# Optimization experiments

Measured on AMD Instinct MI355X. Metric: run time of the kernel, lower is better.

The kernel has to match this reference:

```python
import jax, jax.numpy as jnp
import numpy as np

B, L, DM, H, DK, DV, DH = 16, 1024, 512, 8, 64, 64, 2048
FACTOR = 5
EPS = 1e-5


def _ln(x, g, b):
    m = x.mean(-1, keepdims=True)
    v = jnp.mean((x - m) ** 2, axis=-1, keepdims=True)
    return g * (x - m) / jnp.sqrt(v + EPS) + b


def setup_inputs() -> dict:
    key = jax.random.key(0)
    ks = jax.random.split(key, 12)
    w = lambda k, s: jax.random.normal(k, s, jnp.float32) * 0.02
    sample_k = min(FACTOR * int(np.ceil(np.log(L))), L)  # 35
    return {
        "x": jax.random.normal(ks[0], (B, L, DM), jnp.float32),
        "Wq": w(ks[1], (DM, H * DK)), "bq": jnp.zeros((H * DK,), jnp.float32),
        "Wk": w(ks[2], (DM, H * DK)), "bk": jnp.zeros((H * DK,), jnp.float32),
        "Wv": w(ks[3], (DM, H * DV)), "bv": jnp.zeros((H * DV,), jnp.float32),
        "Wo": w(ks[4], (H * DV, DM)), "bo": jnp.zeros((DM,), jnp.float32),
        "g1": jnp.ones((DM,), jnp.float32), "beta1": jnp.zeros((DM,), jnp.float32),
        "W1": w(ks[5], (DM, DH)), "bf1": jnp.zeros((DH,), jnp.float32),
        "W2": w(ks[6], (DH, DM)), "bf2": jnp.zeros((DM,), jnp.float32),
        "g2": jnp.ones((DM,), jnp.float32), "beta2": jnp.zeros((DM,), jnp.float32),
        "index_sample": jax.random.randint(ks[7], (L, sample_k), 0, L),
        "stage": 0,  # eval; mask=False so attn_mask is always False
    }


def _prob_attention(Q, K, V, index_sample):
    # Q,K,V: [B,H,L,D] (Informer ProbAttention, mask_flag=False, eval)
    Bq, Hq, Lq, D = Q.shape
    u = index_sample.shape[1]  # u == U_part since L_Q == L_K
    # sparse sampled scores: K gathered per-query -> [B,H,L,sample_k,D]
    K_sample = K[:, :, index_sample, :]
    QK_sample = jnp.einsum("bhld,bhlsd->bhls", Q, K_sample)
    M = QK_sample.max(-1) - QK_sample.mean(-1)            # [B,H,L] sparsity measure
    _, M_top = jax.lax.top_k(M, u)                         # [B,H,u]
    Q_reduce = jnp.take_along_axis(Q, M_top[..., None], axis=2)  # [B,H,u,D]
    scores = jnp.einsum("bhud,bhld->bhul", Q_reduce, K) / jnp.sqrt(jnp.float32(D))
    attn = jax.nn.softmax(scores, axis=-1)                 # [B,H,u,L]
    # initial context = mean of V over keys, broadcast to all queries
    context = jnp.broadcast_to(V.mean(axis=2, keepdims=True), V.shape)
    bi = jnp.arange(Bq)[:, None, None]
    hi = jnp.arange(Hq)[None, :, None]
    context = context.at[bi, hi, M_top].set(jnp.einsum("bhul,bhld->bhud", attn, V))
    # output_attention=True: uniform 1/L everywhere, true attn at selected queries
    attns = jnp.full((Bq, Hq, Lq, Lq), 1.0 / Lq, dtype=attn.dtype)
    attns = attns.at[bi, hi, M_top].set(attn)
    return context, attns


def reference(x, Wq, bq, Wk, bk, Wv, bv, Wo, bo, g1, beta1, W1, bf1, W2, bf2, g2, beta2, index_sample, stage):
    residual = x
    Q = (x @ Wq + bq).reshape(B, L, H, DK).transpose(0, 2, 1, 3)
    K = (x @ Wk + bk).reshape(B, L, H, DK).transpose(0, 2, 1, 3)
    V = (x @ Wv + bv).reshape(B, L, H, DV).transpose(0, 2, 1, 3)
    ctx, score = _prob_attention(Q, K, V, index_sample)
    ctx = ctx.transpose(0, 2, 1, 3).reshape(B, L, H * DV)
    out = ctx @ Wo + bo
    x1 = _ln(out + residual, g1, beta1)          # dropout = identity (eval)
    ffn = jax.nn.relu(x1 @ W1 + bf1) @ W2 + bf2
    x2 = _ln(ffn + x1, g2, beta2)
    return x2, score
```

## Files before the change

kernel.cpp:

```cpp
#include <hip/hip_runtime.h>
#include <cstdint>
#include <cstddef>

#define Bc 16
#define Lc 1024
#define DMc 512
#define Hc 8
#define DHc 2048
#define Uc 35

typedef __attribute__((ext_vector_type(8))) short bf16x8;
typedef __attribute__((ext_vector_type(4))) float f32x4;

__device__ __forceinline__ ushort f2bf(float f) {
    union { float f; uint32_t u; } v; v.f = f;
    uint32_t r = v.u + 0x7FFF + ((v.u >> 16) & 1);
    return (ushort)(r >> 16);
}
__device__ __forceinline__ float bf2f(ushort u) {
    union { uint32_t i; float f; } v; v.i = ((uint32_t)u) << 16; return v.f;
}

__device__ __forceinline__ void glds16(const ushort* g, ushort* l) {
    __builtin_amdgcn_global_load_lds(
        (__attribute__((address_space(1))) void*)(void*)const_cast<ushort*>(g),
        (__attribute__((address_space(3))) void*)l, 16, 0, 0);
}

template<int MODE>
__global__ __launch_bounds__(256) void gemm_mfma(
    const ushort* __restrict__ A, const ushort* __restrict__ Bt,
    const float* __restrict__ bias, void* __restrict__ out0,
    void* __restrict__ out1, int M, int N, int K, int nxb)
{
    __shared__ ushort As[2][128 * 64];
    __shared__ ushort Bs[2][128 * 64];
    const int nwg = gridDim.x;
    int wg = blockIdx.x;
    wg = (wg & 7) * (nwg >> 3) + (wg >> 3);
    const int n0 = (wg % nxb) * 128;
    const int m0 = (wg / nxb) * 128;

    const int tid = threadIdx.x;
    const int lane = tid & 63;
    const int wave = tid >> 6;
    const int wr = wave >> 1, wc = wave & 1;
    const int lrow = lane & 15;
    const int lk = (lane >> 4) * 8;

    f32x4 zero = {0.f, 0.f, 0.f, 0.f};
    f32x4 acc[4][4];
    #pragma unroll
    for (int m = 0; m < 4; ++m)
        #pragma unroll
        for (int n = 0; n < 4; ++n) acc[m][n] = zero;

    const int srow = tid >> 3;
    const int skc = (tid & 7) * 8;
    const int ldsb = (tid & 192) * 8;

    auto stage = [&](int k0, int bufi) {
        #pragma unroll
        for (int r = 0; r < 4; ++r) {
            glds16(A  + (size_t)(m0 + r * 32 + srow) * K + k0 + skc, &As[bufi][r * 2048 + ldsb]);
            glds16(Bt + (size_t)(n0 + r * 32 + srow) * K + k0 + skc, &Bs[bufi][r * 2048 + ldsb]);
        }
    };

    const int nt = K >> 6;
    stage(0, 0);
    __syncthreads();
    int cur = 0;
    for (int t = 0; t < nt; ++t) {
        if (t + 1 < nt) stage((t + 1) << 6, cur ^ 1);
        #pragma unroll
        for (int kk = 0; kk < 2; ++kk) {
            bf16x8 af[4], bv[4];
            #pragma unroll
            for (int m = 0; m < 4; ++m)
                af[m] = *reinterpret_cast<const bf16x8*>(&As[cur][(wr * 64 + m * 16 + lrow) * 64 + kk * 32 + lk]);
            #pragma unroll
            for (int n = 0; n < 4; ++n)
                bv[n] = *reinterpret_cast<const bf16x8*>(&Bs[cur][(wc * 64 + n * 16 + lrow) * 64 + kk * 32 + lk]);
            #pragma unroll
            for (int m = 0; m < 4; ++m)
                #pragma unroll
                for (int n = 0; n < 4; ++n)
                    acc[m][n] = __builtin_amdgcn_mfma_f32_16x16x32_bf16(af[m], bv[n], acc[m][n], 0, 0, 0);
        }
        __syncthreads();
        cur ^= 1;
    }

    #pragma unroll
    for (int n = 0; n < 4; ++n) {
        int col = n0 + wc * 64 + n * 16 + lrow;
        float bval = bias[col];
        #pragma unroll
        for (int m = 0; m < 4; ++m) {
            #pragma unroll
            for (int j = 0; j < 4; ++j) {
                int row = m0 + wr * 64 + m * 16 + (lane >> 4) * 4 + j;
                float v = acc[m][n][j] + bval;
                if (MODE == 2) v = fmaxf(v, 0.0f);
                if (MODE == 0)
                    ((float*)out0)[(size_t)row * N + col] = v;
                else if (MODE == 1 || MODE == 2)
                    ((ushort*)out0)[(size_t)row * N + col] = f2bf(v);
                else {
                    if (col < 1024) ((ushort*)out0)[(size_t)row * 1024 + col] = f2bf(v);
                    else            ((float*)out1)[(size_t)row * 512 + (col - 1024)] = v;
                }
            }
        }
    }
}

__device__ __forceinline__ void tr_tile(
    const float* __restrict__ in, ushort* __restrict__ out,
    int K, int N, int bx, int by, float (*t)[33], int tid)
{
    int n0 = bx * 32, k0 = by * 32;
    int tx = tid & 31, ty = tid >> 5;
    #pragma unroll
    for (int dy = 0; dy < 32; dy += 8)
        t[ty + dy][tx] = in[(size_t)(k0 + ty + dy) * N + n0 + tx];
    __syncthreads();
    #pragma unroll
    for (int dy = 0; dy < 32; dy += 8)
        out[(size_t)(n0 + ty + dy) * K + k0 + tx] = f2bf(t[tx][ty + dy]);
}

#define PREP_BLKS (8192 + 4 * 256 + 2 * 1024 + 1)
#define FILL_BLKS 32768

__global__ __launch_bounds__(256) void prep_kernel(
    const float* __restrict__ x,
    const float* __restrict__ Wq, const float* __restrict__ Wk,
    const float* __restrict__ Wv, const float* __restrict__ Wo,
    const float* __restrict__ W1, const float* __restrict__ W2,
    const float* __restrict__ bq, const float* __restrict__ bk,
    const float* __restrict__ bv,
    ushort* __restrict__ xbf, ushort* __restrict__ Wqkvt,
    ushort* __restrict__ Wot, ushort* __restrict__ W1t,
    ushort* __restrict__ W2t, float* __restrict__ bcat,
    float* __restrict__ score_out)
{
    __shared__ float t[32][33];
    const int tid = threadIdx.x;
    int bid = blockIdx.x;
    if (bid < 8192) {
        int i = bid * 256 + tid;
        float4 v = reinterpret_cast<const float4*>(x)[i];
        uint32_t lo = (uint32_t)f2bf(v.x) | ((uint32_t)f2bf(v.y) << 16);
        uint32_t hi = (uint32_t)f2bf(v.z) | ((uint32_t)f2bf(v.w) << 16);
        reinterpret_cast<uint2*>(xbf)[i] = make_uint2(lo, hi);
        return;
    }
    bid -= 8192;
    if (bid < 256) { tr_tile(Wq, Wqkvt,              512, 512, bid & 15, bid >> 4, t, tid); return; }
    bid -= 256;
    if (bid < 256) { tr_tile(Wk, Wqkvt + 512 * 512,  512, 512, bid & 15, bid >> 4, t, tid); return; }
    bid -= 256;
    if (bid < 256) { tr_tile(Wv, Wqkvt + 1024 * 512, 512, 512, bid & 15, bid >> 4, t, tid); return; }
    bid -= 256;
    if (bid < 256) { tr_tile(Wo, Wot,                512, 512, bid & 15, bid >> 4, t, tid); return; }
    bid -= 256;
    if (bid < 1024) { tr_tile(W1, W1t,               512, 2048, bid & 63, bid >> 6, t, tid); return; }
    bid -= 1024;
    if (bid < 1024) { tr_tile(W2, W2t,               2048, 512, bid & 15, bid >> 4, t, tid); return; }
    bid -= 1024;
    if (bid < 1) {
        for (int i = tid; i < 1536; i += 256)
            bcat[i] = (i < 512) ? bq[i] : (i < 1024) ? bk[i - 512] : bv[i - 1024];
        return;
    }
    bid -= 1;
    const float iv = 1.0f / (float)Lc;
    float4 v = make_float4(iv, iv, iv, iv);
    size_t i = (size_t)bid * 256 + tid;
    const size_t nthreads = (size_t)FILL_BLKS * 256;
    float4* p = reinterpret_cast<float4*>(score_out);
    #pragma unroll
    for (int c = 0; c < 4; ++c) p[i + c * nthreads] = v;
}

__global__ __launch_bounds__(256) void compute_M_kernel(
    const ushort* __restrict__ QK, const int* __restrict__ idx,
    float* __restrict__ Mout)
{
    __shared__ float qs[4][64];
    const int tid = threadIdx.x;
    const int wid = tid >> 6;
    const int lane = tid & 63;
    const int task = blockIdx.x * 4 + wid;
    const int l = task & (Lc - 1);
    const int bh = task >> 10;
    const int h = bh & (Hc - 1);
    const int b = bh >> 3;

    qs[wid][lane] = bf2f(QK[(size_t)(b * Lc + l) * 1024 + h * 64 + lane]);

    const bool act = lane < Uc;
    int kl = act ? idx[l * Uc + lane] : 0;
    const bf16x8* kr = reinterpret_cast<const bf16x8*>(
        QK + (size_t)(b * Lc + kl) * 1024 + 512 + h * 64);
    float dot = 0.0f;
    if (act) {
        #pragma unroll
        for (int c = 0; c < 8; ++c) {
            bf16x8 kv = kr[c];
            #pragma unroll
            for (int e = 0; e < 8; ++e)
                dot += qs[wid][c * 8 + e] * bf2f((ushort)kv[e]);
        }
    }
    float mx = act ? dot : -INFINITY;
    float sm = act ? dot : 0.0f;
    #pragma unroll
    for (int off = 32; off; off >>= 1) {
        mx = fmaxf(mx, __shfl_xor(mx, off, 64));
        sm += __shfl_xor(sm, off, 64);
    }
    if (lane == 0) Mout[task] = mx - sm * (1.0f / Uc);
}

__global__ __launch_bounds__(256) void topk_kernel(
    const float* __restrict__ Mvals, int* __restrict__ Mtop)
{
    const int bh = blockIdx.x;
    const int t = threadIdx.x;
    const int lane = t & 63, wid = t >> 6;
    float v[4];
    #pragma unroll
    for (int c = 0; c < 4; ++c) v[c] = Mvals[((size_t)bh << 10) + t + 256 * c];

    __shared__ float cv[4];
    __shared__ int   ci[4];
    __shared__ int   wini;

    for (int j = 0; j < Uc; ++j) {
        float bv = v[0]; int bi = t;
        #pragma unroll
        for (int c = 1; c < 4; ++c)
            if (v[c] > bv) { bv = v[c]; bi = t + 256 * c; }
        #pragma unroll
        for (int off = 32; off; off >>= 1) {
            float ov = __shfl_xor(bv, off, 64);
            int   oi = __shfl_xor(bi, off, 64);
            if (ov > bv || (ov == bv && oi < bi)) { bv = ov; bi = oi; }
        }
        if (lane == 0) { cv[wid] = bv; ci[wid] = bi; }
        __syncthreads();
        if (t == 0) {
            float fv = cv[0]; int fi = ci[0];
            #pragma unroll
            for (int w = 1; w < 4; ++w)
                if (cv[w] > fv || (cv[w] == fv && ci[w] < fi)) { fv = cv[w]; fi = ci[w]; }
            Mtop[bh * Uc + j] = fi;
            wini = fi;
        }
        __syncthreads();
        int wi = wini;
        if ((wi & 255) == t) v[wi >> 8] = -INFINITY;
    }
}

__global__ __launch_bounds__(256) void qk_scores_kernel(
    const ushort* __restrict__ QK, const int* __restrict__ Mtop,
    float* __restrict__ score)
{
    const int bh = blockIdx.x >> 2;
    const int l0 = (blockIdx.x & 3) * 256;
    const int h = bh & (Hc - 1), b = bh >> 3;
    __shared__ int qpos[Uc];
    __shared__ float Qs[Uc][64];
    const int t = threadIdx.x;
    if (t < Uc) qpos[t] = Mtop[bh * Uc + t];
    __syncthreads();
    for (int i = t; i < Uc * 64; i += 256) {
        int j = i >> 6, d = i & 63;
        Qs[j][d] = bf2f(QK[(size_t)(b * Lc + qpos[j]) * 1024 + h * 64 + d]);
    }
    __syncthreads();

    const int l = l0 + t;
    const bf16x8* kr = reinterpret_cast<const bf16x8*>(
        QK + (size_t)(b * Lc + l) * 1024 + 512 + h * 64);
    float acc[Uc] = {};
    #pragma unroll
    for (int c = 0; c < 8; ++c) {
        bf16x8 kv = kr[c];
        float kf[8];
        #pragma unroll
        for (int e = 0; e < 8; ++e) kf[e] = bf2f((ushort)kv[e]);
        #pragma unroll
        for (int j = 0; j < Uc; ++j) {
            float s = 0.0f;
            #pragma unroll
            for (int e = 0; e < 8; ++e) s += Qs[j][c * 8 + e] * kf[e];
            acc[j] += s;
        }
    }
    #pragma unroll
    for (int j = 0; j < Uc; ++j)
        score[((size_t)(bh << 10) + qpos[j]) * Lc + l] = acc[j] * 0.125f;
}

__global__ __launch_bounds__(256) void attn_out_kernel(
    float* __restrict__ score, const float* __restrict__ V,
    const int* __restrict__ Mtop, ushort* __restrict__ ctx)
{
    const int bh = blockIdx.x;
    const int h = bh & (Hc - 1), b = bh >> 3;
    const int t = threadIdx.x;
    const int d = t & 63, part = t >> 6;

    __shared__ int qpos[Uc];
    __shared__ float mz[Uc][2];
    __shared__ float buf[4][Uc][64];
    __shared__ float vmred[4][64];
    __shared__ float vmf[64];

    if (t < Uc) qpos[t] = Mtop[bh * Uc + t];
    __syncthreads();

    for (int j = part; j < Uc; j += 4) {
        const float* row = score + ((size_t)(bh << 10) + qpos[j]) * Lc;
        float v[16];
        float mx = -INFINITY;
        #pragma unroll
        for (int c = 0; c < 16; ++c) { v[c] = row[c * 64 + d]; mx = fmaxf(mx, v[c]); }
        #pragma unroll
        for (int off = 32; off; off >>= 1) mx = fmaxf(mx, __shfl_xor(mx, off, 64));
        float z = 0.0f;
        #pragma unroll
        for (int c = 0; c < 16; ++c) z += expf(v[c] - mx);
        #pragma unroll
        for (int off = 32; off; off >>= 1) z += __shfl_xor(z, off, 64);
        if (d == 0) { mz[j][0] = mx; mz[j][1] = 1.0f / z; }
    }
    __syncthreads();

    float acc[Uc];
    #pragma unroll
    for (int j = 0; j < Uc; ++j) acc[j] = 0.0f;
    float vm = 0.0f;

    for (int c = 0; c < 4; ++c) {
        const int l0 = part * 256 + c * 64;
        #pragma unroll
        for (int j = 0; j < Uc; ++j) {
            size_t off = ((size_t)(bh << 10) + qpos[j]) * Lc + l0 + d;
            float p = expf(score[off] - mz[j][0]) * mz[j][1];
            buf[part][j][d] = p;
            score[off] = p;
        }
        __syncthreads();
        #pragma unroll 4
        for (int li = 0; li < 64; ++li) {
            float v = V[((size_t)(b << 10) + l0 + li) * 512 + h * 64 + d];
            vm += v;
            #pragma unroll
            for (int j = 0; j < Uc; ++j) acc[j] += buf[part][j][li] * v;
        }
        __syncthreads();
    }

    #pragma unroll
    for (int j = 0; j < Uc; ++j) buf[part][j][d] = acc[j];
    vmred[part][d] = vm;
    __syncthreads();
    if (t < 64) vmf[t] = (vmred[0][t] + vmred[1][t] + vmred[2][t] + vmred[3][t]) * (1.0f / Lc);
    __syncthreads();

    const int dcol = (t & 15) * 4;
    ushort4 vmu;
    vmu.x = f2bf(vmf[dcol + 0]); vmu.y = f2bf(vmf[dcol + 1]);
    vmu.z = f2bf(vmf[dcol + 2]); vmu.w = f2bf(vmf[dcol + 3]);
    for (int li = 0; li < 64; ++li) {
        int l = (t >> 4) + li * 16;
        *reinterpret_cast<ushort4*>(ctx + ((size_t)(b << 10) + l) * 512 + h * 64 + dcol) = vmu;
    }
    __syncthreads();

    for (int idx = t; idx < Uc * 64; idx += 256) {
        int j = idx >> 6, d2 = idx & 63;
        float s = buf[0][j][d2] + buf[1][j][d2] + buf[2][j][d2] + buf[3][j][d2];
        ctx[((size_t)(b << 10) + qpos[j]) * 512 + h * 64 + d2] = f2bf(s);
    }
}

template<int A_BF, int B_BF, int OUT_BF>
__global__ __launch_bounds__(256) void ln_kernel(
    const void* __restrict__ a, const void* __restrict__ bsrc,
    const float* __restrict__ g, const float* __restrict__ beta,
    void* __restrict__ y)
{
    const int row = blockIdx.x;
    const int t = threadIdx.x;
    float a0, a1, b0, b1;
    if (A_BF) {
        uint32_t u = ((const uint32_t*)a)[(size_t)row * 256 + t];
        a0 = bf2f((ushort)(u & 0xffff)); a1 = bf2f((ushort)(u >> 16));
    } else {
        float2 f = ((const float2*)a)[(size_t)row * 256 + t];
        a0 = f.x; a1 = f.y;
    }
    if (B_BF) {
        uint32_t u = ((const uint32_t*)bsrc)[(size_t)row * 256 + t];
        b0 = bf2f((ushort)(u & 0xffff)); b1 = bf2f((ushort)(u >> 16));
    } else {
        float2 f = ((const float2*)bsrc)[(size_t)row * 256 + t];
        b0 = f.x; b1 = f.y;
    }
    float v0 = a0 + b0, v1 = a1 + b1;
    __shared__ float red[256];
    red[t] = v0 + v1; __syncthreads();
    for (int s = 128; s; s >>= 1) { if (t < s) red[t] += red[t + s]; __syncthreads(); }
    float mean = red[0] * (1.0f / DMc);
    __syncthreads();
    float d0 = v0 - mean, d1 = v1 - mean;
    red[t] = d0 * d0 + d1 * d1; __syncthreads();
    for (int s = 128; s; s >>= 1) { if (t < s) red[t] += red[t + s]; __syncthreads(); }
    float inv = rsqrtf(red[0] * (1.0f / DMc) + 1e-5f);
    float2 gv = ((const float2*)g)[t];
    float2 bt = ((const float2*)beta)[t];
    float o0 = gv.x * d0 * inv + bt.x;
    float o1 = gv.y * d1 * inv + bt.y;
    if (OUT_BF) {
        uint32_t u = (uint32_t)f2bf(o0) | ((uint32_t)f2bf(o1) << 16);
        ((uint32_t*)y)[(size_t)row * 256 + t] = u;
    } else {
        ((float2*)y)[(size_t)row * 256 + t] = make_float2(o0, o1);
    }
}

extern "C" void kernel_launch(void* const* d_in, const int* in_sizes, int n_in,
                              void* d_out, int out_size, void* d_ws, size_t ws_size,
                              hipStream_t stream)
{
    const float* x     = (const float*)d_in[0];
    const float* Wq    = (const float*)d_in[1];
    const float* bq    = (const float*)d_in[2];
    const float* Wk    = (const float*)d_in[3];
    const float* bk    = (const float*)d_in[4];
    const float* Wv    = (const float*)d_in[5];
    const float* bv    = (const float*)d_in[6];
    const float* Wo    = (const float*)d_in[7];
    const float* bo    = (const float*)d_in[8];
    const float* g1    = (const float*)d_in[9];
    const float* beta1 = (const float*)d_in[10];
    const float* W1    = (const float*)d_in[11];
    const float* bf1   = (const float*)d_in[12];
    const float* W2    = (const float*)d_in[13];
    const float* bf2   = (const float*)d_in[14];
    const float* g2    = (const float*)d_in[15];
    const float* beta2 = (const float*)d_in[16];
    const int* index_sample = (const int*)d_in[17];

    const size_t NTOK = (size_t)Bc * Lc;
    const size_t QKV_SZ = NTOK * DMc;
    const size_t HID_SZ = NTOK * DHc;

    char* p = (char*)d_ws;
    auto alloc = [&](size_t bytes) { char* r = p; p += (bytes + 255) & ~(size_t)255; return r; };
    ushort* QKbf   = (ushort*)alloc(NTOK * 1024 * 2);
    float*  V      = (float*) alloc(QKV_SZ * 4);
    ushort* hidden = (ushort*)alloc(HID_SZ * 2);
    ushort* xbf    = (ushort*)alloc(QKV_SZ * 2);
    ushort* ctxbf  = (ushort*)alloc(QKV_SZ * 2);
    ushort* x1bf   = (ushort*)alloc(QKV_SZ * 2);
    ushort* projbf = (ushort*)alloc(QKV_SZ * 2);
    float*  ffnf   = (float*) alloc(QKV_SZ * 4);
    ushort* Wqkvt  = (ushort*)alloc((size_t)1536 * 512 * 2);
    ushort* Wot    = (ushort*)alloc((size_t)512 * 512 * 2);
    ushort* W1t    = (ushort*)alloc((size_t)512 * 2048 * 2);
    ushort* W2t    = (ushort*)alloc((size_t)512 * 2048 * 2);
    float*  bcat   = (float*) alloc(1536 * 4);
    float*  Mbuf   = (float*) alloc((size_t)Bc * Hc * Lc * 4);
    int*    Mtop   = (int*)   alloc((size_t)Bc * Hc * 64 * 4);

    float* x2_out    = (float*)d_out;
    float* score_out = x2_out + QKV_SZ;

    dim3 blk(256);

    prep_kernel<<<PREP_BLKS + FILL_BLKS, blk, 0, stream>>>(
        x, Wq, Wk, Wv, Wo, W1, W2, bq, bk, bv,
        xbf, Wqkvt, Wot, W1t, W2t, bcat, score_out);

    gemm_mfma<3><<<12 * 128, blk, 0, stream>>>(
        xbf, Wqkvt, bcat, QKbf, V, (int)NTOK, 1536, 512, 12);

    compute_M_kernel<<<(Bc * Hc * Lc) / 4, blk, 0, stream>>>(QKbf, index_sample, Mbuf);
    topk_kernel<<<Bc * Hc, blk, 0, stream>>>(Mbuf, Mtop);

    qk_scores_kernel<<<Bc * Hc * 4, blk, 0, stream>>>(QKbf, Mtop, score_out);
    attn_out_kernel<<<Bc * Hc, blk, 0, stream>>>(score_out, V, Mtop, ctxbf);

    gemm_mfma<1><<<4 * 128, blk, 0, stream>>>(
        ctxbf, Wot, bo, projbf, nullptr, (int)NTOK, 512, 512, 4);
    ln_kernel<1, 0, 1><<<(int)NTOK, blk, 0, stream>>>(projbf, x, g1, beta1, x1bf);

    gemm_mfma<2><<<16 * 128, blk, 0, stream>>>(
        x1bf, W1t, bf1, hidden, nullptr, (int)NTOK, 2048, 512, 16);
    gemm_mfma<0><<<4 * 128, blk, 0, stream>>>(
        hidden, W2t, bf2, ffnf, nullptr, (int)NTOK, 512, 2048, 4);
    ln_kernel<0, 1, 0><<<(int)NTOK, blk, 0, stream>>>(ffnf, x1bf, g2, beta2, x2_out);
}
```

Measured before the change: 667.6 us.

## Fuse QK scores, softmax and AV into one kernel; store V as bf16

The separate score and attention-output kernels become one 1024-thread block per (batch, head). It computes the selected-query scores, does the softmax in registers and writes the probabilities once, then multiplies by V in groups of five queries. This removes the score write, re-read and rewrite pass. V now comes out of the QKV GEMM as bf16 in a single packed buffer, which halves V traffic but lowers its precision. The GEMM K-tile is also cut from 64 to 32, giving half the LDS and more barriers per tile.

```diff
diff --git a/kernel.cpp b/kernel.cpp
--- a/kernel.cpp
+++ b/kernel.cpp
@@ -31,10 +31,10 @@
 __global__ __launch_bounds__(256) void gemm_mfma(
     const ushort* __restrict__ A, const ushort* __restrict__ Bt,
     const float* __restrict__ bias, void* __restrict__ out0,
-    void* __restrict__ out1, int M, int N, int K, int nxb)
-{
-    __shared__ ushort As[2][128 * 64];
-    __shared__ ushort Bs[2][128 * 64];
+    int M, int N, int K, int nxb)
+{
+    __shared__ ushort As[2][128 * 32];
+    __shared__ ushort Bs[2][128 * 32];
     const int nwg = gridDim.x;
     int wg = blockIdx.x;
     wg = (wg & 7) * (nwg >> 3) + (wg >> 3);
@@ -55,39 +55,35 @@
         #pragma unroll
         for (int n = 0; n < 4; ++n) acc[m][n] = zero;
 
-    const int srow = tid >> 3;
-    const int skc = (tid & 7) * 8;
+    const int srow = tid >> 2;
+    const int skc = (tid & 3) * 8;
     const int ldsb = (tid & 192) * 8;
 
     auto stage = [&](int k0, int bufi) {
-        #pragma unroll
-        for (int r = 0; r < 4; ++r) {
-            glds16(A  + (size_t)(m0 + r * 32 + srow) * K + k0 + skc, &As[bufi][r * 2048 + ldsb]);
-            glds16(Bt + (size_t)(n0 + r * 32 + srow) * K + k0 + skc, &Bs[bufi][r * 2048 + ldsb]);
-        }
+        glds16(A  + (size_t)(m0 + srow) * K + k0 + skc,      &As[bufi][ldsb]);
+        glds16(A  + (size_t)(m0 + 64 + srow) * K + k0 + skc, &As[bufi][2048 + ldsb]);
+        glds16(Bt + (size_t)(n0 + srow) * K + k0 + skc,      &Bs[bufi][ldsb]);
+        glds16(Bt + (size_t)(n0 + 64 + srow) * K + k0 + skc, &Bs[bufi][2048 + ldsb]);
     };
 
-    const int nt = K >> 6;
+    const int nt = K >> 5;
     stage(0, 0);
     __syncthreads();
     int cur = 0;
     for (int t = 0; t < nt; ++t) {
-        if (t + 1 < nt) stage((t + 1) << 6, cur ^ 1);
-        #pragma unroll
-        for (int kk = 0; kk < 2; ++kk) {
-            bf16x8 af[4], bv[4];
-            #pragma unroll
-            for (int m = 0; m < 4; ++m)
-                af[m] = *reinterpret_cast<const bf16x8*>(&As[cur][(wr * 64 + m * 16 + lrow) * 64 + kk * 32 + lk]);
+        if (t + 1 < nt) stage((t + 1) << 5, cur ^ 1);
+        bf16x8 af[4], bv[4];
+        #pragma unroll
+        for (int m = 0; m < 4; ++m)
+            af[m] = *reinterpret_cast<const bf16x8*>(&As[cur][(wr * 64 + m * 16 + lrow) * 32 + lk]);
+        #pragma unroll
+        for (int n = 0; n < 4; ++n)
+            bv[n] = *reinterpret_cast<const bf16x8*>(&Bs[cur][(wc * 64 + n * 16 + lrow) * 32 + lk]);
+        #pragma unroll
+        for (int m = 0; m < 4; ++m)
             #pragma unroll
             for (int n = 0; n < 4; ++n)
-                bv[n] = *reinterpret_cast<const bf16x8*>(&Bs[cur][(wc * 64 + n * 16 + lrow) * 64 + kk * 32 + lk]);
-            #pragma unroll
-            for (int m = 0; m < 4; ++m)
-                #pragma unroll
-                for (int n = 0; n < 4; ++n)
-                    acc[m][n] = __builtin_amdgcn_mfma_f32_16x16x32_bf16(af[m], bv[n], acc[m][n], 0, 0, 0);
-        }
+                acc[m][n] = __builtin_amdgcn_mfma_f32_16x16x32_bf16(af[m], bv[n], acc[m][n], 0, 0, 0);
         __syncthreads();
         cur ^= 1;
     }
@@ -105,12 +101,8 @@
                 if (MODE == 2) v = fmaxf(v, 0.0f);
                 if (MODE == 0)
                     ((float*)out0)[(size_t)row * N + col] = v;
-                else if (MODE == 1 || MODE == 2)
+                else
                     ((ushort*)out0)[(size_t)row * N + col] = f2bf(v);
-                else {
-                    if (col < 1024) ((ushort*)out0)[(size_t)row * 1024 + col] = f2bf(v);
-                    else            ((float*)out1)[(size_t)row * 512 + (col - 1024)] = v;
-                }
             }
         }
     }
@@ -186,7 +178,7 @@
 }
 
 __global__ __launch_bounds__(256) void compute_M_kernel(
-    const ushort* __restrict__ QK, const int* __restrict__ idx,
+    const ushort* __restrict__ QKV, const int* __restrict__ idx,
     float* __restrict__ Mout)
 {
     __shared__ float qs[4][64];
@@ -199,12 +191,12 @@
     const int h = bh & (Hc - 1);
     const int b = bh >> 3;
 
-    qs[wid][lane] = bf2f(QK[(size_t)(b * Lc + l) * 1024 + h * 64 + lane]);
+    qs[wid][lane] = bf2f(QKV[(size_t)(b * Lc + l) * 1536 + h * 64 + lane]);
 
     const bool act = lane < Uc;
     int kl = act ? idx[l * Uc + lane] : 0;
     const bf16x8* kr = reinterpret_cast<const bf16x8*>(
-        QK + (size_t)(b * Lc + kl) * 1024 + 512 + h * 64);
+        QKV + (size_t)(b * Lc + kl) * 1536 + 512 + h * 64);
     float dot = 0.0f;
     if (act) {
         #pragma unroll
@@ -266,28 +258,40 @@
     }
 }
 
-__global__ __launch_bounds__(256) void qk_scores_kernel(
-    const ushort* __restrict__ QK, const int* __restrict__ Mtop,
-    float* __restrict__ score)
-{
-    const int bh = blockIdx.x >> 2;
-    const int l0 = (blockIdx.x & 3) * 256;
+#define JG 5
+__global__ __launch_bounds__(1024) void fused_attn_kernel(
+    const ushort* __restrict__ QKV, const int* __restrict__ Mtop,
+    float* __restrict__ score, ushort* __restrict__ ctx)
+{
+    const int bh = blockIdx.x;
     const int h = bh & (Hc - 1), b = bh >> 3;
+    const int t = threadIdx.x;
+    const int lane = t & 63, wid = t >> 6;
+
+    __shared__ float pA[JG][Lc];
+    __shared__ float pB[16][JG][64];
+    __shared__ float pv[Uc][64];
+    __shared__ float red16[16][Uc];
+    __shared__ float mz[Uc][2];
+    __shared__ float vmred[16][64];
+    __shared__ float vmf[64];
     __shared__ int qpos[Uc];
-    __shared__ float Qs[Uc][64];
-    const int t = threadIdx.x;
+
+    float* Qs = &pA[0][0];
+
     if (t < Uc) qpos[t] = Mtop[bh * Uc + t];
     __syncthreads();
-    for (int i = t; i < Uc * 64; i += 256) {
+    for (int i = t; i < Uc * 64; i += 1024) {
         int j = i >> 6, d = i & 63;
-        Qs[j][d] = bf2f(QK[(size_t)(b * Lc + qpos[j]) * 1024 + h * 64 + d]);
-    }
-    __syncthreads();
-
-    const int l = l0 + t;
+        Qs[i] = bf2f(QKV[(size_t)(b * Lc + qpos[j]) * 1536 + h * 64 + d]);
+    }
+    __syncthreads();
+
     const bf16x8* kr = reinterpret_cast<const bf16x8*>(
-        QK + (size_t)(b * Lc + l) * 1024 + 512 + h * 64);
-    float acc[Uc] = {};
+        QKV + (size_t)(b * Lc + t) * 1536 + 512 + h * 64);
+    float s[Uc];
+    #pragma unroll
+    for (int j = 0; j < Uc; ++j) s[j] = 0.0f;
     #pragma unroll
     for (int c = 0; c < 8; ++c) {
         bf16x8 kv = kr[c];
@@ -296,98 +300,104 @@
         for (int e = 0; e < 8; ++e) kf[e] = bf2f((ushort)kv[e]);
         #pragma unroll
         for (int j = 0; j < Uc; ++j) {
-            float s = 0.0f;
-            #pragma unroll
-            for (int e = 0; e < 8; ++e) s += Qs[j][c * 8 + e] * kf[e];
-            acc[j] += s;
-        }
-    }
-    #pragma unroll
-    for (int j = 0; j < Uc; ++j)
-        score[((size_t)(bh << 10) + qpos[j]) * Lc + l] = acc[j] * 0.125f;
-}
-
-__global__ __launch_bounds__(256) void attn_out_kernel(
-    float* __restrict__ score, const float* __restrict__ V,
-    const int* __restrict__ Mtop, ushort* __restrict__ ctx)
-{
-    const int bh = blockIdx.x;
-    const int h = bh & (Hc - 1), b = bh >> 3;
-    const int t = threadIdx.x;
+            float a = 0.0f;
+            #pragma unroll
+            for (int e = 0; e < 8; ++e) a += Qs[j * 64 + c * 8 + e] * kf[e];
+            s[j] += a;
+        }
+    }
+    #pragma unroll
+    for (int j = 0; j < Uc; ++j) s[j] *= 0.125f;
+    __syncthreads();
+
+    #pragma unroll
+    for (int j = 0; j < Uc; ++j) {
+        float m = s[j];
+        #pragma unroll
+        for (int off = 32; off; off >>= 1) m = fmaxf(m, __shfl_xor(m, off, 64));
+        if (lane == 0) red16[wid][j] = m;
+    }
+    __syncthreads();
+    if (t < Uc) {
+        float m = red16[0][t];
+        #pragma unroll
+        for (int w = 1; w < 16; ++w) m = fmaxf(m, red16[w][t]);
+        mz[t][0] = m;
+    }
+    __syncthreads();
+    #pragma unroll
+    for (int j = 0; j < Uc; ++j) {
+        s[j] = expf(s[j] - mz[j][0]);
+        float z = s[j];
+        #pragma unroll
+        for (int off = 32; off; off >>= 1) z += __shfl_xor(z, off, 64);
+        if (lane == 0) red16[wid][j] = z;
+    }
+    __syncthreads();
+    if (t < Uc) {
+        float z = red16[0][t];
+        #pragma unroll
+        for (int w = 1; w < 16; ++w) z += red16[w][t];
+        mz[t][1] = 1.0f / z;
+    }
+    __syncthreads();
+
+    #pragma unroll
+    for (int j = 0; j < Uc; ++j) {
+        s[j] *= mz[j][1];
+        score[((size_t)(bh << 10) + qpos[j]) * Lc + t] = s[j];
+    }
+
     const int d = t & 63, part = t >> 6;
-
-    __shared__ int qpos[Uc];
-    __shared__ float mz[Uc][2];
-    __shared__ float buf[4][Uc][64];
-    __shared__ float vmred[4][64];
-    __shared__ float vmf[64];
-
-    if (t < Uc) qpos[t] = Mtop[bh * Uc + t];
-    __syncthreads();
-
-    for (int j = part; j < Uc; j += 4) {
-        const float* row = score + ((size_t)(bh << 10) + qpos[j]) * Lc;
-        float v[16];
-        float mx = -INFINITY;
-        #pragma unroll
-        for (int c = 0; c < 16; ++c) { v[c] = row[c * 64 + d]; mx = fmaxf(mx, v[c]); }
-        #pragma unroll
-        for (int off = 32; off; off >>= 1) mx = fmaxf(mx, __shfl_xor(mx, off, 64));
-        float z = 0.0f;
-        #pragma unroll
-        for (int c = 0; c < 16; ++c) z += expf(v[c] - mx);
-        #pragma unroll
-        for (int off = 32; off; off >>= 1) z += __shfl_xor(z, off, 64);
-        if (d == 0) { mz[j][0] = mx; mz[j][1] = 1.0f / z; }
-    }
-    __syncthreads();
-
-    float acc[Uc];
-    #pragma unroll
-    for (int j = 0; j < Uc; ++j) acc[j] = 0.0f;
-    float vm = 0.0f;
-
-    for (int c = 0; c < 4; ++c) {
-        const int l0 = part * 256 + c * 64;
-        #pragma unroll
-        for (int j = 0; j < Uc; ++j) {
-            size_t off = ((size_t)(bh << 10) + qpos[j]) * Lc + l0 + d;
-            float p = expf(score[off] - mz[j][0]) * mz[j][1];
-            buf[part][j][d] = p;
-            score[off] = p;
-        }
+    for (int g = 0; g < 7; ++g) {
         __syncthreads();
+        #pragma unroll
+        for (int jg = 0; jg < JG; ++jg) pA[jg][t] = s[g * JG + jg];
+        __syncthreads();
+        float acc[JG] = {};
+        float vm = 0.0f;
         #pragma unroll 4
         for (int li = 0; li < 64; ++li) {
-            float v = V[((size_t)(b << 10) + l0 + li) * 512 + h * 64 + d];
+            int l = part * 64 + li;
+            float v = bf2f(QKV[(size_t)(b * Lc + l) * 1536 + 1024 + h * 64 + d]);
             vm += v;
             #pragma unroll
-            for (int j = 0; j < Uc; ++j) acc[j] += buf[part][j][li] * v;
-        }
+            for (int jg = 0; jg < JG; ++jg) acc[jg] += pA[jg][l] * v;
+        }
+        #pragma unroll
+        for (int jg = 0; jg < JG; ++jg) pB[part][jg][d] = acc[jg];
+        if (g == 0) vmred[part][d] = vm;
         __syncthreads();
-    }
-
-    #pragma unroll
-    for (int j = 0; j < Uc; ++j) buf[part][j][d] = acc[j];
-    vmred[part][d] = vm;
-    __syncthreads();
-    if (t < 64) vmf[t] = (vmred[0][t] + vmred[1][t] + vmred[2][t] + vmred[3][t]) * (1.0f / Lc);
+        if (t < JG * 64) {
+            int jj = t >> 6, d2 = t & 63;
+            float ssum = 0.0f;
+            #pragma unroll
+            for (int w = 0; w < 16; ++w) ssum += pB[w][jj][d2];
+            pv[g * JG + jj][d2] = ssum;
+        }
+    }
+    __syncthreads();
+    if (t < 64) {
+        float m = 0.0f;
+        #pragma unroll
+        for (int w = 0; w < 16; ++w) m += vmred[w][t];
+        vmf[t] = m * (1.0f / Lc);
+    }
     __syncthreads();
 
     const int dcol = (t & 15) * 4;
     ushort4 vmu;
     vmu.x = f2bf(vmf[dcol + 0]); vmu.y = f2bf(vmf[dcol + 1]);
     vmu.z = f2bf(vmf[dcol + 2]); vmu.w = f2bf(vmf[dcol + 3]);
-    for (int li = 0; li < 64; ++li) {
-        int l = (t >> 4) + li * 16;
-        *reinterpret_cast<ushort4*>(ctx + ((size_t)(b << 10) + l) * 512 + h * 64 + dcol) = vmu;
-    }
-    __syncthreads();
-
-    for (int idx = t; idx < Uc * 64; idx += 256) {
-        int j = idx >> 6, d2 = idx & 63;
-        float s = buf[0][j][d2] + buf[1][j][d2] + buf[2][j][d2] + buf[3][j][d2];
-        ctx[((size_t)(b << 10) + qpos[j]) * 512 + h * 64 + d2] = f2bf(s);
+    #pragma unroll 4
+    for (int it = 0; it < 16; ++it) {
+        int row = (t >> 4) + it * 64;
+        *reinterpret_cast<ushort4*>(ctx + ((size_t)(b << 10) + row) * 512 + h * 64 + dcol) = vmu;
+    }
+    __syncthreads();
+    for (int i = t; i < Uc * 64; i += 1024) {
+        int j = i >> 6, d2 = i & 63;
+        ctx[((size_t)(b << 10) + qpos[j]) * 512 + h * 64 + d2] = f2bf(pv[j][d2]);
     }
 }
 
@@ -465,8 +475,7 @@
 
     char* p = (char*)d_ws;
     auto alloc = [&](size_t bytes) { char* r = p; p += (bytes + 255) & ~(size_t)255; return r; };
-    ushort* QKbf   = (ushort*)alloc(NTOK * 1024 * 2);
-    float*  V      = (float*) alloc(QKV_SZ * 4);
+    ushort* QKVbf  = (ushort*)alloc(NTOK * 1536 * 2);
     ushort* hidden = (ushort*)alloc(HID_SZ * 2);
     ushort* xbf    = (ushort*)alloc(QKV_SZ * 2);
     ushort* ctxbf  = (ushort*)alloc(QKV_SZ * 2);
@@ -490,22 +499,22 @@
         x, Wq, Wk, Wv, Wo, W1, W2, bq, bk, bv,
         xbf, Wqkvt, Wot, W1t, W2t, bcat, score_out);
 
-    gemm_mfma<3><<<12 * 128, blk, 0, stream>>>(
-        xbf, Wqkvt, bcat, QKbf, V, (int)NTOK, 1536, 512, 12);
-
-    compute_M_kernel<<<(Bc * Hc * Lc) / 4, blk, 0, stream>>>(QKbf, index_sample, Mbuf);
+    gemm_mfma<1><<<12 * 128, blk, 0, stream>>>(
+        xbf, Wqkvt, bcat, QKVbf, (int)NTOK, 1536, 512, 12);
+
+    compute_M_kernel<<<(Bc * Hc * Lc) / 4, blk, 0, stream>>>(QKVbf, index_sample, Mbuf);
     topk_kernel<<<Bc * Hc, blk, 0, stream>>>(Mbuf, Mtop);
 
-    qk_scores_kernel<<<Bc * Hc * 4, blk, 0, stream>>>(QKbf, Mtop, score_out);
-    attn_out_kernel<<<Bc * Hc, blk, 0, stream>>>(score_out, V, Mtop, ctxbf);
+    fused_attn_kernel<<<Bc * Hc, dim3(1024), 0, stream>>>(
+        QKVbf, Mtop, score_out, ctxbf);
 
     gemm_mfma<1><<<4 * 128, blk, 0, stream>>>(
-        ctxbf, Wot, bo, projbf, nullptr, (int)NTOK, 512, 512, 4);
+        ctxbf, Wot, bo, projbf, (int)NTOK, 512, 512, 4);
     ln_kernel<1, 0, 1><<<(int)NTOK, blk, 0, stream>>>(projbf, x, g1, beta1, x1bf);
 
     gemm_mfma<2><<<16 * 128, blk, 0, stream>>>(
-        x1bf, W1t, bf1, hidden, nullptr, (int)NTOK, 2048, 512, 16);
+        x1bf, W1t, bf1, hidden, (int)NTOK, 2048, 512, 16);
     gemm_mfma<0><<<4 * 128, blk, 0, stream>>>(
-        hidden, W2t, bf2, ffnf, nullptr, (int)NTOK, 512, 2048, 4);
+        hidden, W2t, bf2, ffnf, (int)NTOK, 512, 2048, 4);
     ln_kernel<0, 1, 0><<<(int)NTOK, blk, 0, stream>>>(ffnf, x1bf, g2, beta2, x2_out);
 }
```

Result: slower. 1.179 ms (+76.5%).

## Halve GEMM K-tile to 32 and store V as bf16 in fused QKV buffer

Applied to the files above, without the earlier changes.

The GEMM's LDS K-tile shrinks from 64 to 32. This halves shared memory per block, which may raise occupancy, but doubles the number of barrier-separated iterations. The QKV projection now writes all three outputs as bf16 into one 1536-wide buffer, so V is no longer kept in fp32. The attention kernels read V from that bf16 buffer with a new stride, cutting V traffic in exchange for lower precision of V.

```diff
diff --git a/kernel.cpp b/kernel.cpp
--- a/kernel.cpp
+++ b/kernel.cpp
@@ -31,10 +31,10 @@
 __global__ __launch_bounds__(256) void gemm_mfma(
     const ushort* __restrict__ A, const ushort* __restrict__ Bt,
     const float* __restrict__ bias, void* __restrict__ out0,
-    void* __restrict__ out1, int M, int N, int K, int nxb)
-{
-    __shared__ ushort As[2][128 * 64];
-    __shared__ ushort Bs[2][128 * 64];
+    int M, int N, int K, int nxb)
+{
+    __shared__ ushort As[2][128 * 32];
+    __shared__ ushort Bs[2][128 * 32];
     const int nwg = gridDim.x;
     int wg = blockIdx.x;
     wg = (wg & 7) * (nwg >> 3) + (wg >> 3);
@@ -55,39 +55,35 @@
         #pragma unroll
         for (int n = 0; n < 4; ++n) acc[m][n] = zero;
 
-    const int srow = tid >> 3;
-    const int skc = (tid & 7) * 8;
+    const int srow = tid >> 2;
+    const int skc = (tid & 3) * 8;
     const int ldsb = (tid & 192) * 8;
 
     auto stage = [&](int k0, int bufi) {
-        #pragma unroll
-        for (int r = 0; r < 4; ++r) {
-            glds16(A  + (size_t)(m0 + r * 32 + srow) * K + k0 + skc, &As[bufi][r * 2048 + ldsb]);
-            glds16(Bt + (size_t)(n0 + r * 32 + srow) * K + k0 + skc, &Bs[bufi][r * 2048 + ldsb]);
-        }
+        glds16(A  + (size_t)(m0 + srow) * K + k0 + skc,      &As[bufi][ldsb]);
+        glds16(A  + (size_t)(m0 + 64 + srow) * K + k0 + skc, &As[bufi][2048 + ldsb]);
+        glds16(Bt + (size_t)(n0 + srow) * K + k0 + skc,      &Bs[bufi][ldsb]);
+        glds16(Bt + (size_t)(n0 + 64 + srow) * K + k0 + skc, &Bs[bufi][2048 + ldsb]);
     };
 
-    const int nt = K >> 6;
+    const int nt = K >> 5;
     stage(0, 0);
     __syncthreads();
     int cur = 0;
     for (int t = 0; t < nt; ++t) {
-        if (t + 1 < nt) stage((t + 1) << 6, cur ^ 1);
-        #pragma unroll
-        for (int kk = 0; kk < 2; ++kk) {
-            bf16x8 af[4], bv[4];
-            #pragma unroll
-            for (int m = 0; m < 4; ++m)
-                af[m] = *reinterpret_cast<const bf16x8*>(&As[cur][(wr * 64 + m * 16 + lrow) * 64 + kk * 32 + lk]);
+        if (t + 1 < nt) stage((t + 1) << 5, cur ^ 1);
+        bf16x8 af[4], bv[4];
+        #pragma unroll
+        for (int m = 0; m < 4; ++m)
+            af[m] = *reinterpret_cast<const bf16x8*>(&As[cur][(wr * 64 + m * 16 + lrow) * 32 + lk]);
+        #pragma unroll
+        for (int n = 0; n < 4; ++n)
+            bv[n] = *reinterpret_cast<const bf16x8*>(&Bs[cur][(wc * 64 + n * 16 + lrow) * 32 + lk]);
+        #pragma unroll
+        for (int m = 0; m < 4; ++m)
             #pragma unroll
             for (int n = 0; n < 4; ++n)
-                bv[n] = *reinterpret_cast<const bf16x8*>(&Bs[cur][(wc * 64 + n * 16 + lrow) * 64 + kk * 32 + lk]);
-            #pragma unroll
-            for (int m = 0; m < 4; ++m)
-                #pragma unroll
-                for (int n = 0; n < 4; ++n)
-                    acc[m][n] = __builtin_amdgcn_mfma_f32_16x16x32_bf16(af[m], bv[n], acc[m][n], 0, 0, 0);
-        }
+                acc[m][n] = __builtin_amdgcn_mfma_f32_16x16x32_bf16(af[m], bv[n], acc[m][n], 0, 0, 0);
         __syncthreads();
         cur ^= 1;
     }
@@ -105,12 +101,8 @@
                 if (MODE == 2) v = fmaxf(v, 0.0f);
                 if (MODE == 0)
                     ((float*)out0)[(size_t)row * N + col] = v;
-                else if (MODE == 1 || MODE == 2)
+                else
                     ((ushort*)out0)[(size_t)row * N + col] = f2bf(v);
-                else {
-                    if (col < 1024) ((ushort*)out0)[(size_t)row * 1024 + col] = f2bf(v);
-                    else            ((float*)out1)[(size_t)row * 512 + (col - 1024)] = v;
-                }
             }
         }
     }
@@ -186,7 +178,7 @@
 }
 
 __global__ __launch_bounds__(256) void compute_M_kernel(
-    const ushort* __restrict__ QK, const int* __restrict__ idx,
+    const ushort* __restrict__ QKV, const int* __restrict__ idx,
     float* __restrict__ Mout)
 {
     __shared__ float qs[4][64];
@@ -199,12 +191,12 @@
     const int h = bh & (Hc - 1);
     const int b = bh >> 3;
 
-    qs[wid][lane] = bf2f(QK[(size_t)(b * Lc + l) * 1024 + h * 64 + lane]);
+    qs[wid][lane] = bf2f(QKV[(size_t)(b * Lc + l) * 1536 + h * 64 + lane]);
 
     const bool act = lane < Uc;
     int kl = act ? idx[l * Uc + lane] : 0;
     const bf16x8* kr = reinterpret_cast<const bf16x8*>(
-        QK + (size_t)(b * Lc + kl) * 1024 + 512 + h * 64);
+        QKV + (size_t)(b * Lc + kl) * 1536 + 512 + h * 64);
     float dot = 0.0f;
     if (act) {
         #pragma unroll
@@ -267,7 +259,7 @@
 }
 
 __global__ __launch_bounds__(256) void qk_scores_kernel(
-    const ushort* __restrict__ QK, const int* __restrict__ Mtop,
+    const ushort* __restrict__ QKV, const int* __restrict__ Mtop,
     float* __restrict__ score)
 {
     const int bh = blockIdx.x >> 2;
@@ -280,13 +272,13 @@
     __syncthreads();
     for (int i = t; i < Uc * 64; i += 256) {
         int j = i >> 6, d = i & 63;
-        Qs[j][d] = bf2f(QK[(size_t)(b * Lc + qpos[j]) * 1024 + h * 64 + d]);
+        Qs[j][d] = bf2f(QKV[(size_t)(b * Lc + qpos[j]) * 1536 + h * 64 + d]);
     }
     __syncthreads();
 
     const int l = l0 + t;
     const bf16x8* kr = reinterpret_cast<const bf16x8*>(
-        QK + (size_t)(b * Lc + l) * 1024 + 512 + h * 64);
+        QKV + (size_t)(b * Lc + l) * 1536 + 512 + h * 64);
     float acc[Uc] = {};
     #pragma unroll
     for (int c = 0; c < 8; ++c) {
@@ -308,7 +300,7 @@
 }
 
 __global__ __launch_bounds__(256) void attn_out_kernel(
-    float* __restrict__ score, const float* __restrict__ V,
+    float* __restrict__ score, const ushort* __restrict__ QKV,
     const int* __restrict__ Mtop, ushort* __restrict__ ctx)
 {
     const int bh = blockIdx.x;
@@ -359,7 +351,7 @@
         __syncthreads();
         #pragma unroll 4
         for (int li = 0; li < 64; ++li) {
-            float v = V[((size_t)(b << 10) + l0 + li) * 512 + h * 64 + d];
+            float v = bf2f(QKV[((size_t)(b << 10) + l0 + li) * 1536 + 1024 + h * 64 + d]);
             vm += v;
             #pragma unroll
             for (int j = 0; j < Uc; ++j) acc[j] += buf[part][j][li] * v;
@@ -465,8 +457,7 @@
 
     char* p = (char*)d_ws;
     auto alloc = [&](size_t bytes) { char* r = p; p += (bytes + 255) & ~(size_t)255; return r; };
-    ushort* QKbf   = (ushort*)alloc(NTOK * 1024 * 2);
-    float*  V      = (float*) alloc(QKV_SZ * 4);
+    ushort* QKVbf  = (ushort*)alloc(NTOK * 1536 * 2);
     ushort* hidden = (ushort*)alloc(HID_SZ * 2);
     ushort* xbf    = (ushort*)alloc(QKV_SZ * 2);
     ushort* ctxbf  = (ushort*)alloc(QKV_SZ * 2);
@@ -490,22 +481,22 @@
         x, Wq, Wk, Wv, Wo, W1, W2, bq, bk, bv,
         xbf, Wqkvt, Wot, W1t, W2t, bcat, score_out);
 
-    gemm_mfma<3><<<12 * 128, blk, 0, stream>>>(
-        xbf, Wqkvt, bcat, QKbf, V, (int)NTOK, 1536, 512, 12);
-
-    compute_M_kernel<<<(Bc * Hc * Lc) / 4, blk, 0, stream>>>(QKbf, index_sample, Mbuf);
+    gemm_mfma<1><<<12 * 128, blk, 0, stream>>>(
+        xbf, Wqkvt, bcat, QKVbf, (int)NTOK, 1536, 512, 12);
+
+    compute_M_kernel<<<(Bc * Hc * Lc) / 4, blk, 0, stream>>>(QKVbf, index_sample, Mbuf);
     topk_kernel<<<Bc * Hc, blk, 0, stream>>>(Mbuf, Mtop);
 
-    qk_scores_kernel<<<Bc * Hc * 4, blk, 0, stream>>>(QKbf, Mtop, score_out);
-    attn_out_kernel<<<Bc * Hc, blk, 0, stream>>>(score_out, V, Mtop, ctxbf);
+    qk_scores_kernel<<<Bc * Hc * 4, blk, 0, stream>>>(QKVbf, Mtop, score_out);
+    attn_out_kernel<<<Bc * Hc, blk, 0, stream>>>(score_out, QKVbf, Mtop, ctxbf);
 
     gemm_mfma<1><<<4 * 128, blk, 0, stream>>>(
-        ctxbf, Wot, bo, projbf, nullptr, (int)NTOK, 512, 512, 4);
+        ctxbf, Wot, bo, projbf, (int)NTOK, 512, 512, 4);
     ln_kernel<1, 0, 1><<<(int)NTOK, blk, 0, stream>>>(projbf, x, g1, beta1, x1bf);
 
     gemm_mfma<2><<<16 * 128, blk, 0, stream>>>(
-        x1bf, W1t, bf1, hidden, nullptr, (int)NTOK, 2048, 512, 16);
+        x1bf, W1t, bf1, hidden, (int)NTOK, 2048, 512, 16);
     gemm_mfma<0><<<4 * 128, blk, 0, stream>>>(
-        hidden, W2t, bf2, ffnf, nullptr, (int)NTOK, 512, 2048, 4);
+        hidden, W2t, bf2, ffnf, (int)NTOK, 512, 2048, 4);
     ln_kernel<0, 1, 0><<<(int)NTOK, blk, 0, stream>>>(ffnf, x1bf, g2, beta2, x2_out);
 }
```

After: 643.4 us. 3.6% less time.
